# Kernel optimization log

Hardware: AMD Instinct MI355X
Metric: run time of the kernel (lower is better)

Reference implementation:

```python
import jax, jax.numpy as jnp
import numpy as np

GRID = 5
ELEMS = GRID * GRID  # 25 values per puzzle grid


def _dup_count(rows):
    """rows: [B, 5, 5]; counts, per row, elements equal to an earlier element
    in the same row (i.e. 5 - num_unique per row, summed). Returns scalar."""
    # eq[b, i, j, k] = rows[b, i, j] == rows[b, i, k]
    eq = rows[:, :, :, None] == rows[:, :, None, :]
    # strictly-lower mask over (j, k): only k < j counts as 'seen earlier'
    earlier = jnp.tril(jnp.ones((GRID, GRID), dtype=bool), k=-1)
    dup = jnp.any(eq & earlier, axis=-1)  # [B, 5, 5]
    return jnp.sum(dup.astype(jnp.float32))


def setup_inputs() -> dict:
    key = jax.random.key(0)
    k1, k2 = jax.random.split(key)
    n = 26214400  # 1,048,576 grids * 25
    preds = jax.random.normal(k1, (n,), dtype=jnp.float32)
    targets = jax.random.randint(k2, (n,), 0, 6, dtype=jnp.int32)
    return {"preds": preds, "targets": targets}


def reference(preds, targets):
    preds_flat = preds.reshape(-1)
    # loss1: mean absolute error against float-cast integer targets
    loss1 = jnp.mean(jnp.abs(preds_flat - targets.astype(jnp.float32)))

    batch_size = targets.shape[0] // ELEMS
    # duplicate counting runs on detached predictions (original uses .detach().cpu().numpy())
    grids = jax.lax.stop_gradient(preds_flat).reshape(batch_size, GRID, GRID)
    total_dup = _dup_count(grids) + _dup_count(jnp.swapaxes(grids, 1, 2))
    loss2 = total_dup / batch_size * 0.1

    # out-of-bounds penalty: .any().item() has no gradient path
    p = jax.lax.stop_gradient(preds_flat)
    oob = jnp.any((p < 0.5) | (p > 5.5))
    return loss1 + loss2 + jnp.where(oob, jnp.float32(1000.0), jnp.float32(0.0))
```

## Files before the change

### kernel.cpp

```cpp
#include <hip/hip_runtime.h>


#define BLOCK 320
#define GRIDS_PER_BLOCK 256
#define ELEMS_PER_BLOCK (GRIDS_PER_BLOCK * 25)
#define VEC_ITERS (ELEMS_PER_BLOCK / 4 / BLOCK)
#define NWAVES (BLOCK / 64)
#define CHUNK_FLOATS 256

#define GLOBAL_AS(p) ((__attribute__((address_space(1))) void*)(p))
#define LDS_AS(p)    ((__attribute__((address_space(3))) void*)(p))

__device__ __forceinline__ int grid_dups(const float* __restrict__ g) {
    int ldup = 0;
    #pragma unroll
    for (int r = 0; r < 5; ++r) {
        const float a = g[r*5+0], b = g[r*5+1], c = g[r*5+2],
                    d = g[r*5+3], e = g[r*5+4];
        ldup += (int)(b == a);
        ldup += (int)((c == a) | (c == b));
        ldup += (int)((d == a) | (d == b) | (d == c));
        ldup += (int)((e == a) | (e == b) | (e == c) | (e == d));
    }
    #pragma unroll
    for (int q = 0; q < 5; ++q) {
        const float a = g[q +  0], b = g[q +  5], c = g[q + 10],
                    d = g[q + 15], e = g[q + 20];
        ldup += (int)(b == a);
        ldup += (int)((c == a) | (c == b));
        ldup += (int)((d == a) | (d == b) | (d == c));
        ldup += (int)((e == a) | (e == b) | (e == c) | (e == d));
    }
    return ldup;
}

__global__ __launch_bounds__(BLOCK) void puzzle_main(
    const float* __restrict__ preds, const int* __restrict__ tgts,
    long long n_total,
    float* __restrict__ blk_sum, int* __restrict__ blk_dup,
    int* __restrict__ blk_oob)
{
    __shared__ float lds[ELEMS_PER_BLOCK];
    __shared__ float s_sum[NWAVES];
    __shared__ int   s_dup[NWAVES];
    __shared__ int   s_oob[NWAVES];

    const int tid  = threadIdx.x;
    const int lane = tid & 63;
    const int wv   = tid >> 6;
    const long long base = (long long)blockIdx.x * ELEMS_PER_BLOCK;
    const long long rem = n_total - base;
    const int nelem = (int)(rem < ELEMS_PER_BLOCK ? rem : ELEMS_PER_BLOCK);

    float lsum = 0.0f;
    int   loob = 0;
    int   ldup = 0;

    if (nelem == ELEMS_PER_BLOCK) {
        const float* src = preds + base;
        const int4* __restrict__ t4 = (const int4*)(tgts + base);

        #pragma unroll
        for (int j = 0; j < 5; ++j) {
            const int off = (wv * 5 + j) * CHUNK_FLOATS;
            __builtin_amdgcn_global_load_lds(GLOBAL_AS(src + off + lane * 4),
                                             LDS_AS(&lds[off]), 16, 0, 0);
        }

        int4 t[VEC_ITERS];
        #pragma unroll
        for (int k = 0; k < VEC_ITERS; ++k) t[k] = t4[tid + k * BLOCK];

        __syncthreads();

        const float4* lds4 = reinterpret_cast<const float4*>(lds);
        #pragma unroll
        for (int k = 0; k < VEC_ITERS; ++k) {
            const float4 p = lds4[tid + k * BLOCK];
            lsum += fabsf(p.x - (float)t[k].x);
            lsum += fabsf(p.y - (float)t[k].y);
            lsum += fabsf(p.z - (float)t[k].z);
            lsum += fabsf(p.w - (float)t[k].w);
            loob |= (int)((p.x < 0.5f) | (p.x > 5.5f));
            loob |= (int)((p.y < 0.5f) | (p.y > 5.5f));
            loob |= (int)((p.z < 0.5f) | (p.z > 5.5f));
            loob |= (int)((p.w < 0.5f) | (p.w > 5.5f));
        }

        if (tid < GRIDS_PER_BLOCK) ldup = grid_dups(&lds[tid * 25]);
    } else {
        const int nvec = nelem >> 2;
        const float4* __restrict__ p4g = (const float4*)(preds + base);
        const int4*   __restrict__ t4g = (const int4*)(tgts + base);
        float4* lds4w = reinterpret_cast<float4*>(lds);
        for (int i = tid; i < nvec; i += BLOCK) {
            const float4 p = p4g[i];
            const int4   t = t4g[i];
            lsum += fabsf(p.x - (float)t.x) + fabsf(p.y - (float)t.y) +
                    fabsf(p.z - (float)t.z) + fabsf(p.w - (float)t.w);
            loob |= (int)((p.x < 0.5f) | (p.x > 5.5f));
            loob |= (int)((p.y < 0.5f) | (p.y > 5.5f));
            loob |= (int)((p.z < 0.5f) | (p.z > 5.5f));
            loob |= (int)((p.w < 0.5f) | (p.w > 5.5f));
            lds4w[i] = p;
        }
        for (int i = (nvec << 2) + tid; i < nelem; i += BLOCK) {
            const float p = preds[base + i];
            const int   t = tgts[base + i];
            lsum += fabsf(p - (float)t);
            loob |= (int)((p < 0.5f) | (p > 5.5f));
            lds[i] = p;
        }
        __syncthreads();
        const int ngrids = nelem / 25;
        if (tid < ngrids) ldup = grid_dups(&lds[tid * 25]);
    }

    #pragma unroll
    for (int off = 32; off > 0; off >>= 1) {
        lsum += __shfl_down(lsum, off, 64);
        ldup += __shfl_down(ldup, off, 64);
        loob |= __shfl_down(loob, off, 64);
    }
    if (lane == 0) { s_sum[wv] = lsum; s_dup[wv] = ldup; s_oob[wv] = loob; }
    __syncthreads();
    if (tid == 0) {
        float bs = 0.0f; int bd = 0, bo = 0;
        #pragma unroll
        for (int w = 0; w < NWAVES; ++w) { bs += s_sum[w]; bd += s_dup[w]; bo |= s_oob[w]; }
        blk_sum[blockIdx.x] = bs;
        blk_dup[blockIdx.x] = bd;
        blk_oob[blockIdx.x] = bo;
    }
}

#define FBLOCK 256
#define FNWAVES (FBLOCK / 64)

__global__ __launch_bounds__(FBLOCK) void puzzle_final(
    const float* __restrict__ blk_sum, const int* __restrict__ blk_dup,
    const int* __restrict__ blk_oob, int nblocks,
    long long n_total, long long batch, float* __restrict__ out)
{
    __shared__ double s_sum[FNWAVES];
    __shared__ int    s_dup[FNWAVES];
    __shared__ int    s_oob[FNWAVES];

    double lsum = 0.0;
    int ldup = 0, loob = 0;
    for (int i = threadIdx.x; i < nblocks; i += FBLOCK) {
        lsum += (double)blk_sum[i];
        ldup += blk_dup[i];
        loob |= blk_oob[i];
    }
    #pragma unroll
    for (int off = 32; off > 0; off >>= 1) {
        lsum += __shfl_down(lsum, off, 64);
        ldup += __shfl_down(ldup, off, 64);
        loob |= __shfl_down(loob, off, 64);
    }
    const int wave = threadIdx.x >> 6;
    if ((threadIdx.x & 63) == 0) { s_sum[wave] = lsum; s_dup[wave] = ldup; s_oob[wave] = loob; }
    __syncthreads();
    if (threadIdx.x == 0) {
        double bs = 0.0; int bd = 0, bo = 0;
        #pragma unroll
        for (int w = 0; w < FNWAVES; ++w) { bs += s_sum[w]; bd += s_dup[w]; bo |= s_oob[w]; }
        const float loss1 = (float)(bs / (double)n_total);
        const float loss2 = (float)((double)bd * 0.1 / (double)batch);
        out[0] = loss1 + loss2 + (bo ? 1000.0f : 0.0f);
    }
}

extern "C" void kernel_launch(void* const* d_in, const int* in_sizes, int n_in,
                              void* d_out, int out_size, void* d_ws, size_t ws_size,
                              hipStream_t stream) {
    const float* preds = (const float*)d_in[0];
    const int*   tgts  = (const int*)d_in[1];
    float* out = (float*)d_out;

    const long long n = (long long)in_sizes[0];
    const long long batch = n / 25;
    const int nblocks = (int)((n + ELEMS_PER_BLOCK - 1) / ELEMS_PER_BLOCK);

    float* blk_sum = (float*)d_ws;
    int*   blk_dup = (int*)(blk_sum + nblocks);
    int*   blk_oob = (int*)(blk_dup + nblocks);

    puzzle_main<<<nblocks, BLOCK, 0, stream>>>(preds, tgts, n,
                                               blk_sum, blk_dup, blk_oob);
    puzzle_final<<<1, FBLOCK, 0, stream>>>(blk_sum, blk_dup, blk_oob,
                                           nblocks, n, batch, out);
}
```

Measured before the change: 225.5 us.

## Use persistent per-wave tiles with async LDS loads of preds and targets

Replaces the one-block-per-256-grids launch with a fixed 512-block persistent grid in which each wave loops over 1600-element tiles (64 grids). Both preds and targets are copied into per-wave LDS with global_load_lds, and each lane then reads one whole grid into registers to compute MAE, min/max and duplicates. This removes block-level syncs and per-block launch overhead, and the out-of-bounds flag is now derived from a min/max reduction. In exchange there is no double buffering, so each wave stalls on its own loads, and the strided LDS reads (25-float stride per lane) may cause bank conflicts.

Measured after the change: 221.9 us. No clear change (-1.6%).

```diff
diff --git a/kernel.cpp b/kernel.cpp
--- a/kernel.cpp
+++ b/kernel.cpp
@@ -1,22 +1,21 @@
 #include <hip/hip_runtime.h>
 
 
-#define BLOCK 320
-#define GRIDS_PER_BLOCK 256
-#define ELEMS_PER_BLOCK (GRIDS_PER_BLOCK * 25)
-#define VEC_ITERS (ELEMS_PER_BLOCK / 4 / BLOCK)
-#define NWAVES (BLOCK / 64)
-#define CHUNK_FLOATS 256
+#define BLOCK 256
+#define WAVES_PER_BLOCK 4
+#define TILE 1600
+#define NBLOCKS 512
+#define NWAVES WAVES_PER_BLOCK
 
 #define GLOBAL_AS(p) ((__attribute__((address_space(1))) void*)(p))
 #define LDS_AS(p)    ((__attribute__((address_space(3))) void*)(p))
 
-__device__ __forceinline__ int grid_dups(const float* __restrict__ g) {
+__device__ __forceinline__ int grid_dups_reg(const float* p) {
     int ldup = 0;
     #pragma unroll
     for (int r = 0; r < 5; ++r) {
-        const float a = g[r*5+0], b = g[r*5+1], c = g[r*5+2],
-                    d = g[r*5+3], e = g[r*5+4];
+        const float a = p[r*5+0], b = p[r*5+1], c = p[r*5+2],
+                    d = p[r*5+3], e = p[r*5+4];
         ldup += (int)(b == a);
         ldup += (int)((c == a) | (c == b));
         ldup += (int)((d == a) | (d == b) | (d == c));
@@ -24,8 +23,8 @@
     }
     #pragma unroll
     for (int q = 0; q < 5; ++q) {
-        const float a = g[q +  0], b = g[q +  5], c = g[q + 10],
-                    d = g[q + 15], e = g[q + 20];
+        const float a = p[q+0], b = p[q+5], c = p[q+10],
+                    d = p[q+15], e = p[q+20];
         ldup += (int)(b == a);
         ldup += (int)((c == a) | (c == b));
         ldup += (int)((d == a) | (d == b) | (d == c));
@@ -40,7 +39,8 @@
     float* __restrict__ blk_sum, int* __restrict__ blk_dup,
     int* __restrict__ blk_oob)
 {
-    __shared__ float lds[ELEMS_PER_BLOCK];
+    __shared__ float lds_p[WAVES_PER_BLOCK * TILE];
+    __shared__ int   lds_t[WAVES_PER_BLOCK * TILE];
     __shared__ float s_sum[NWAVES];
     __shared__ int   s_dup[NWAVES];
     __shared__ int   s_oob[NWAVES];
@@ -48,81 +48,87 @@
     const int tid  = threadIdx.x;
     const int lane = tid & 63;
     const int wv   = tid >> 6;
-    const long long base = (long long)blockIdx.x * ELEMS_PER_BLOCK;
-    const long long rem = n_total - base;
-    const int nelem = (int)(rem < ELEMS_PER_BLOCK ? rem : ELEMS_PER_BLOCK);
+
+    const long long total_tiles = n_total / TILE;
+    const int total_waves = gridDim.x * WAVES_PER_BLOCK;
+    const int gwave = blockIdx.x * WAVES_PER_BLOCK + wv;
+
+    float* __restrict__ wp = &lds_p[wv * TILE];
+    int*   __restrict__ wt = &lds_t[wv * TILE];
 
     float lsum = 0.0f;
-    int   loob = 0;
     int   ldup = 0;
+    float mn =  1e30f;
+    float mx = -1e30f;
 
-    if (nelem == ELEMS_PER_BLOCK) {
-        const float* src = preds + base;
-        const int4* __restrict__ t4 = (const int4*)(tgts + base);
+    for (long long t = gwave; t < total_tiles; t += total_waves) {
+        const float* srcp = preds + t * TILE;
+        const int*   srct = tgts  + t * TILE;
+
+        __builtin_amdgcn_sched_barrier(0);
+        #pragma unroll
+        for (int c = 0; c < 6; ++c)
+            __builtin_amdgcn_global_load_lds(GLOBAL_AS(srcp + c*256 + lane*4),
+                                             LDS_AS(wp + c*256), 16, 0, 0);
+        __builtin_amdgcn_global_load_lds(GLOBAL_AS(srcp + 1536 + lane),
+                                         LDS_AS(wp + 1536), 4, 0, 0);
+        #pragma unroll
+        for (int c = 0; c < 6; ++c)
+            __builtin_amdgcn_global_load_lds(GLOBAL_AS(srct + c*256 + lane*4),
+                                             LDS_AS(wt + c*256), 16, 0, 0);
+        __builtin_amdgcn_global_load_lds(GLOBAL_AS(srct + 1536 + lane),
+                                         LDS_AS(wt + 1536), 4, 0, 0);
+
+        __builtin_amdgcn_s_waitcnt(0x0F70);
+        __builtin_amdgcn_sched_barrier(0);
+
+        const float* __restrict__ g  = wp + lane * 25;
+        const int*   __restrict__ ti = wt + lane * 25;
+
+        float p[25];
+        #pragma unroll
+        for (int j = 0; j < 25; ++j) p[j] = g[j];
 
         #pragma unroll
-        for (int j = 0; j < 5; ++j) {
-            const int off = (wv * 5 + j) * CHUNK_FLOATS;
-            __builtin_amdgcn_global_load_lds(GLOBAL_AS(src + off + lane * 4),
-                                             LDS_AS(&lds[off]), 16, 0, 0);
+        for (int j = 0; j < 25; ++j) {
+            lsum += fabsf(p[j] - (float)ti[j]);
+            mn = fminf(mn, p[j]);
+            mx = fmaxf(mx, p[j]);
         }
+        ldup += grid_dups_reg(p);
+    }
 
-        int4 t[VEC_ITERS];
-        #pragma unroll
-        for (int k = 0; k < VEC_ITERS; ++k) t[k] = t4[tid + k * BLOCK];
-
-        __syncthreads();
-
-        const float4* lds4 = reinterpret_cast<const float4*>(lds);
-        #pragma unroll
-        for (int k = 0; k < VEC_ITERS; ++k) {
-            const float4 p = lds4[tid + k * BLOCK];
-            lsum += fabsf(p.x - (float)t[k].x);
-            lsum += fabsf(p.y - (float)t[k].y);
-            lsum += fabsf(p.z - (float)t[k].z);
-            lsum += fabsf(p.w - (float)t[k].w);
-            loob |= (int)((p.x < 0.5f) | (p.x > 5.5f));
-            loob |= (int)((p.y < 0.5f) | (p.y > 5.5f));
-            loob |= (int)((p.z < 0.5f) | (p.z > 5.5f));
-            loob |= (int)((p.w < 0.5f) | (p.w > 5.5f));
+    const long long rem = n_total - total_tiles * TILE;
+    if (rem > 0 && gwave == total_waves - 1) {
+        const int ngrids = (int)(rem / 25);
+        if (lane < ngrids) {
+            const float* srcp = preds + total_tiles * TILE + (long long)lane * 25;
+            const int*   srct = tgts  + total_tiles * TILE + (long long)lane * 25;
+            float p[25];
+            #pragma unroll
+            for (int j = 0; j < 25; ++j) p[j] = srcp[j];
+            #pragma unroll
+            for (int j = 0; j < 25; ++j) {
+                lsum += fabsf(p[j] - (float)srct[j]);
+                mn = fminf(mn, p[j]);
+                mx = fmaxf(mx, p[j]);
+            }
+            ldup += grid_dups_reg(p);
         }
-
-        if (tid < GRIDS_PER_BLOCK) ldup = grid_dups(&lds[tid * 25]);
-    } else {
-        const int nvec = nelem >> 2;
-        const float4* __restrict__ p4g = (const float4*)(preds + base);
-        const int4*   __restrict__ t4g = (const int4*)(tgts + base);
-        float4* lds4w = reinterpret_cast<float4*>(lds);
-        for (int i = tid; i < nvec; i += BLOCK) {
-            const float4 p = p4g[i];
-            const int4   t = t4g[i];
-            lsum += fabsf(p.x - (float)t.x) + fabsf(p.y - (float)t.y) +
-                    fabsf(p.z - (float)t.z) + fabsf(p.w - (float)t.w);
-            loob |= (int)((p.x < 0.5f) | (p.x > 5.5f));
-            loob |= (int)((p.y < 0.5f) | (p.y > 5.5f));
-            loob |= (int)((p.z < 0.5f) | (p.z > 5.5f));
-            loob |= (int)((p.w < 0.5f) | (p.w > 5.5f));
-            lds4w[i] = p;
-        }
-        for (int i = (nvec << 2) + tid; i < nelem; i += BLOCK) {
-            const float p = preds[base + i];
-            const int   t = tgts[base + i];
-            lsum += fabsf(p - (float)t);
-            loob |= (int)((p < 0.5f) | (p > 5.5f));
-            lds[i] = p;
-        }
-        __syncthreads();
-        const int ngrids = nelem / 25;
-        if (tid < ngrids) ldup = grid_dups(&lds[tid * 25]);
     }
 
     #pragma unroll
     for (int off = 32; off > 0; off >>= 1) {
         lsum += __shfl_down(lsum, off, 64);
         ldup += __shfl_down(ldup, off, 64);
-        loob |= __shfl_down(loob, off, 64);
+        mn = fminf(mn, __shfl_down(mn, off, 64));
+        mx = fmaxf(mx, __shfl_down(mx, off, 64));
     }
-    if (lane == 0) { s_sum[wv] = lsum; s_dup[wv] = ldup; s_oob[wv] = loob; }
+    if (lane == 0) {
+        s_sum[wv] = lsum;
+        s_dup[wv] = ldup;
+        s_oob[wv] = (int)((mn < 0.5f) | (mx > 5.5f));
+    }
     __syncthreads();
     if (tid == 0) {
         float bs = 0.0f; int bd = 0, bo = 0;
@@ -181,14 +187,13 @@
 
     const long long n = (long long)in_sizes[0];
     const long long batch = n / 25;
-    const int nblocks = (int)((n + ELEMS_PER_BLOCK - 1) / ELEMS_PER_BLOCK);
 
     float* blk_sum = (float*)d_ws;
-    int*   blk_dup = (int*)(blk_sum + nblocks);
-    int*   blk_oob = (int*)(blk_dup + nblocks);
+    int*   blk_dup = (int*)(blk_sum + NBLOCKS);
+    int*   blk_oob = (int*)(blk_dup + NBLOCKS);
 
-    puzzle_main<<<nblocks, BLOCK, 0, stream>>>(preds, tgts, n,
+    puzzle_main<<<NBLOCKS, BLOCK, 0, stream>>>(preds, tgts, n,
                                                blk_sum, blk_dup, blk_oob);
     puzzle_final<<<1, FBLOCK, 0, stream>>>(blk_sum, blk_dup, blk_oob,
-                                           nblocks, n, batch, out);
+                                           NBLOCKS, n, batch, out);
 }
```
